# Optimization experiments

Measured on AMD Instinct MI355X. Metric: run time of the kernel, lower is better.

## Reference

```python
import jax, jax.numpy as jnp
import numpy as np

B, N, M = 4, 1024, 3072          # batch, latent (query) len, prefix context len
D, H, DH, L, F = 512, 8, 64, 6, 2048  # dim, heads, dim_head, depth, ff hidden
SCALE = DH ** -0.5


def _ln(x, g, b):
    m = jnp.mean(x, axis=-1, keepdims=True)
    v = jnp.mean(jnp.square(x - m), axis=-1, keepdims=True)
    return (x - m) * jax.lax.rsqrt(v + 1e-5) * g + b


def _heads(t):  # [b, n, h*d] -> [b, h, n, d]
    b, n, _ = t.shape
    return t.reshape(b, n, H, DH).transpose(0, 2, 1, 3)


def _attend(q, k, v):
    # q:[b,h,i,d], k/v:[b,h,j,d]; causal mask triu(j-i+1) as in source
    i, j = q.shape[2], k.shape[2]
    sim = jnp.einsum('bhid,bhjd->bhij', q * SCALE, k)
    mask = jnp.triu(jnp.ones((i, j), dtype=bool), j - i + 1)
    sim = jnp.where(mask, -jnp.finfo(sim.dtype).max, sim)
    attn = jax.nn.softmax(sim, axis=-1)
    out = jnp.einsum('bhij,bhjd->bhid', attn, v)
    return out.transpose(0, 2, 1, 3).reshape(q.shape[0], i, H * DH)


def _ff(x, g, b, w1, w2):
    return jax.nn.gelu(_ln(x, g, b) @ w1, approximate=False) @ w2


def setup_inputs() -> dict:
    key = jax.random.key(0)
    ks = jax.random.split(key, 12)
    rn = lambda k, shape: jax.random.normal(k, shape, dtype=jnp.float32) * 0.02
    return {
        'x': jax.random.normal(ks[0], (B, N, D), jnp.float32),
        'context': jax.random.normal(ks[1], (B, M, D), jnp.float32),
        'pa_norm_g': jnp.ones((D,), jnp.float32), 'pa_norm_b': jnp.zeros((D,), jnp.float32),
        'pa_cnorm_g': jnp.ones((D,), jnp.float32), 'pa_cnorm_b': jnp.zeros((D,), jnp.float32),
        'pa_wq': rn(ks[2], (D, H * DH)), 'pa_wkv': rn(ks[3], (D, 2 * H * DH)),
        'pa_wo': rn(ks[4], (H * DH, D)), 'pa_wo_b': jnp.zeros((D,), jnp.float32),
        'pf_ln_g': jnp.ones((D,), jnp.float32), 'pf_ln_b': jnp.zeros((D,), jnp.float32),
        'pf_w1': rn(ks[5], (D, F)), 'pf_w2': rn(ks[6], (F, D)),
        'sa_ln_g': jnp.ones((L, D), jnp.float32), 'sa_ln_b': jnp.zeros((L, D), jnp.float32),
        'sa_wqkv': rn(ks[7], (L, D, 3 * H * DH)), 'sa_wo': rn(ks[8], (L, H * DH, D)),
        'sf_ln_g': jnp.ones((L, D), jnp.float32), 'sf_ln_b': jnp.zeros((L, D), jnp.float32),
        'sf_w1': rn(ks[9], (L, D, F)), 'sf_w2': rn(ks[10], (L, F, D)),
    }


def reference(x, context, pa_norm_g, pa_norm_b, pa_cnorm_g, pa_cnorm_b,
              pa_wq, pa_wkv, pa_wo, pa_wo_b, pf_ln_g, pf_ln_b, pf_w1, pf_w2,
              sa_ln_g, sa_ln_b, sa_wqkv, sa_wo, sf_ln_g, sf_ln_b, sf_w1, sf_w2):
    # --- CausalPrefixAttention (eval mode: no dropout, context_mask=None) ---
    xn = _ln(x, pa_norm_g, pa_norm_b)
    cn = _ln(context, pa_cnorm_g, pa_cnorm_b)
    q = _heads(xn @ pa_wq)
    k_in, v_in = jnp.split(xn @ pa_wkv, 2, axis=-1)
    k_c, v_c = jnp.split(cn @ pa_wkv, 2, axis=-1)
    k = _heads(jnp.concatenate([k_c, k_in], axis=1))  # [b,h,M+N,d]
    v = _heads(jnp.concatenate([v_c, v_in], axis=1))
    x = _attend(q, k, v) @ pa_wo + pa_wo_b + x
    x = _ff(x, pf_ln_g, pf_ln_b, pf_w1, pf_w2) + x
    # --- depth x (CausalAttention + FeedForward) ---
    for l in range(L):
        xn = _ln(x, sa_ln_g[l], sa_ln_b[l])
        qq, kk, vv = jnp.split(xn @ sa_wqkv[l], 3, axis=-1)
        x = _attend(_heads(qq), _heads(kk), _heads(vv)) @ sa_wo[l] + x
        x = _ff(x, sf_ln_g[l], sf_ln_b[l], sf_w1[l], sf_w2[l]) + x
    return x
```

## Files before the change

### kernel.cpp

```cpp
#include <hip/hip_runtime.h>
#include <hip/hip_bf16.h>
#include <cstdint>
#include <cstddef>

typedef __bf16 bf16;
typedef __attribute__((ext_vector_type(8))) __bf16 bf16x8;
typedef __attribute__((ext_vector_type(4))) __bf16 bf16x4;
typedef __attribute__((ext_vector_type(4))) float f32x4;

constexpr int B_ = 4, QN = 1024, MCTX = 3072, D_ = 512, H_ = 8, DHE = 64, L_ = 6, FF_ = 2048;
constexpr float SCALE_ = 0.125f;

__device__ __forceinline__ f32x4 mfma16(bf16x8 a, bf16x8 b, f32x4 c) {
  return __builtin_amdgcn_mfma_f32_16x16x32_bf16(a, b, c, 0, 0, 0);
}

__device__ __forceinline__ void gl_lds16(const bf16* g, bf16* l) {
  __builtin_amdgcn_global_load_lds((const __attribute__((address_space(1))) void*)g,
                                   (__attribute__((address_space(3))) void*)l, 16, 0, 0);
}

__global__ __launch_bounds__(256) void ln_kernel(const float* __restrict__ x,
                                                 const float* __restrict__ g,
                                                 const float* __restrict__ b,
                                                 bf16* __restrict__ out, int rows) {
  int wid = threadIdx.x >> 6, lane = threadIdx.x & 63;
  int row = blockIdx.x * 4 + wid;
  if (row >= rows) return;
  const float* xr = x + (size_t)row * D_;
  f32x4 a0 = *(const f32x4*)(xr + lane * 8);
  f32x4 a1 = *(const f32x4*)(xr + lane * 8 + 4);
  float s = 0.f;
#pragma unroll
  for (int i = 0; i < 4; i++) { s += a0[i]; s += a1[i]; }
#pragma unroll
  for (int d = 1; d < 64; d <<= 1) s += __shfl_xor(s, d);
  float mean = s * (1.0f / 512.0f);
  float q = 0.f;
#pragma unroll
  for (int i = 0; i < 4; i++) {
    float t0 = a0[i] - mean, t1 = a1[i] - mean;
    q += t0 * t0 + t1 * t1;
  }
#pragma unroll
  for (int d = 1; d < 64; d <<= 1) q += __shfl_xor(q, d);
  float rstd = rsqrtf(q * (1.0f / 512.0f) + 1e-5f);
  f32x4 g0 = *(const f32x4*)(g + lane * 8);
  f32x4 g1 = *(const f32x4*)(g + lane * 8 + 4);
  f32x4 b0 = *(const f32x4*)(b + lane * 8);
  f32x4 b1 = *(const f32x4*)(b + lane * 8 + 4);
  bf16x8 o;
#pragma unroll
  for (int i = 0; i < 4; i++) {
    o[i] = (bf16)((a0[i] - mean) * rstd * g0[i] + b0[i]);
    o[i + 4] = (bf16)((a1[i] - mean) * rstd * g1[i] + b1[i]);
  }
  *(bf16x8*)(out + (size_t)row * D_ + lane * 8) = o;
}

struct WDesc { const float* src; bf16* dst; int K; int N; int tstart; };
struct WPack { WDesc d[30]; int n; };

__global__ __launch_bounds__(256) void wtrans_all(WPack p) {
  __shared__ float tile[64][65];
  const int bid = blockIdx.x;
  int mi = 0;
  for (int i = 1; i < p.n; i++)
    if (p.d[i].tstart <= bid) mi = i;
  const float* src = p.d[mi].src;
  bf16* dst = p.d[mi].dst;
  const int K = p.d[mi].K, N = p.d[mi].N;
  const int lt = bid - p.d[mi].tstart;
  const int ntx = N >> 6;
  const int n0 = (lt % ntx) * 64, k0 = (lt / ntx) * 64;
  const int tx = threadIdx.x, ty = threadIdx.y;
#pragma unroll
  for (int pp = 0; pp < 16; pp++)
    tile[pp * 4 + ty][tx] = src[(size_t)(k0 + pp * 4 + ty) * N + n0 + tx];
  __syncthreads();
#pragma unroll
  for (int pp = 0; pp < 16; pp++)
    dst[(size_t)(n0 + pp * 4 + ty) * K + k0 + tx] = (bf16)tile[tx][pp * 4 + ty];
}

__global__ __launch_bounds__(256) void vtrans_kernel(const bf16* __restrict__ src,
                                                     bf16* __restrict__ vt,
                                                     int Skv, int rstride, int coloff) {
  __shared__ bf16 tile[64][65];
  int tx = threadIdx.x, ty = threadIdx.y;
  int s0 = blockIdx.x * 64, h = blockIdx.y, b = blockIdx.z;
  const bf16* sp = src + (size_t)b * Skv * rstride + coloff + h * 64;
#pragma unroll
  for (int p = 0; p < 16; p++)
    tile[p * 4 + ty][tx] = sp[(size_t)(s0 + p * 4 + ty) * rstride + tx];
  __syncthreads();
  bf16* op = vt + ((size_t)(b * H_ + h) * 64) * Skv;
#pragma unroll
  for (int p = 0; p < 16; p++)
    op[(size_t)(p * 4 + ty) * Skv + s0 + tx] = tile[tx][p * 4 + ty];
}

template <int EPI>
__global__ __launch_bounds__(256) void gemm128(const bf16* __restrict__ A,
                                               const bf16* __restrict__ BT,
                                               void* __restrict__ Cout,
                                               const float* __restrict__ resid,
                                               const float* __restrict__ bias,
                                               int M, int N, int K,
                                               int rpbi, int rpbo, int roff) {
  __shared__ bf16 smA[2][128 * 64];
  __shared__ bf16 smB[2][128 * 64];
  const int tid = threadIdx.x, wid = tid >> 6, lane = tid & 63;
  const int lr = lane & 15, lg = lane >> 4;
  const int tm = blockIdx.y * 128, tn = blockIdx.x * 128;
  const int wr = (wid >> 1) * 64, wc = (wid & 1) * 64;

  const int l3 = lane >> 3;
  const int kslot = ((lane & 7) ^ l3) * 8;
  const bf16* gA[4];
  const bf16* gB[4];
#pragma unroll
  for (int j = 0; j < 4; j++) {
    gA[j] = A + (size_t)(tm + wid * 32 + j * 8 + l3) * K + kslot;
    gB[j] = BT + (size_t)(tn + wid * 32 + j * 8 + l3) * K + kslot;
  }

  f32x4 acc[4][4] = {};
  const int nt = K >> 6;

  auto stage = [&](int bi, int kt) {
#pragma unroll
    for (int j = 0; j < 4; j++) {
      gl_lds16(gA[j] + kt, &smA[bi][(wid * 32 + j * 8) * 64]);
      gl_lds16(gB[j] + kt, &smB[bi][(wid * 32 + j * 8) * 64]);
    }
  };

  stage(0, 0);
  int buf = 0;
  for (int t = 0; t < nt; ++t) {
    asm volatile("s_waitcnt vmcnt(0)" ::: "memory");
    __builtin_amdgcn_s_barrier();
    __builtin_amdgcn_sched_barrier(0);
    if (t + 1 < nt) stage(buf ^ 1, (t + 1) * 64);

    bf16x8 af[4][2], bfr[4][2];
#pragma unroll
    for (int i = 0; i < 4; i++) {
      const int row = wr + i * 16 + lr;
#pragma unroll
      for (int kk = 0; kk < 2; kk++)
        af[i][kk] = *(const bf16x8*)(&smA[buf][row * 64 + (((kk * 4 + lg) ^ (row & 7)) * 8)]);
    }
#pragma unroll
    for (int j = 0; j < 4; j++) {
      const int row = wc + j * 16 + lr;
#pragma unroll
      for (int kk = 0; kk < 2; kk++)
        bfr[j][kk] = *(const bf16x8*)(&smB[buf][row * 64 + (((kk * 4 + lg) ^ (row & 7)) * 8)]);
    }
#pragma unroll
    for (int kk = 0; kk < 2; kk++)
#pragma unroll
      for (int i = 0; i < 4; i++)
#pragma unroll
        for (int j = 0; j < 4; j++)
          acc[i][j] = mfma16(af[i][kk], bfr[j][kk], acc[i][j]);
    buf ^= 1;
  }

#pragma unroll
  for (int i = 0; i < 4; i++) {
#pragma unroll
    for (int r = 0; r < 4; r++) {
      int row = tm + wr + i * 16 + lg * 4 + r;
      int orow = (row / rpbi) * rpbo + (row % rpbi) + roff;
#pragma unroll
      for (int j = 0; j < 4; j++) {
        int col = tn + wc + j * 16 + lr;
        float v = acc[i][j][r];
        if (EPI == 0) {
          ((bf16*)Cout)[(size_t)orow * N + col] = (bf16)v;
        } else if (EPI == 1) {
          float gv = 0.5f * v * (1.0f + erff(v * 0.70710678118f));
          ((bf16*)Cout)[(size_t)orow * N + col] = (bf16)gv;
        } else {
          if (bias) v += bias[col];
          v += resid[(size_t)orow * N + col];
          ((float*)Cout)[(size_t)orow * N + col] = v;
        }
      }
    }
  }
}

template <int EPI>
__global__ __launch_bounds__(256) void gemm64(const bf16* __restrict__ A,
                                              const bf16* __restrict__ BT,
                                              void* __restrict__ Cout,
                                              const float* __restrict__ resid,
                                              const float* __restrict__ bias,
                                              int M, int N, int K,
                                              int rpbi, int rpbo, int roff) {
  __shared__ bf16 smA[3][64 * 64];
  __shared__ bf16 smB[3][64 * 64];
  const int tid = threadIdx.x, wid = tid >> 6, lane = tid & 63;
  const int lr = lane & 15, lg = lane >> 4;
  const int tm = blockIdx.y * 64, tn = blockIdx.x * 64;
  const int wr = (wid >> 1) * 32, wc = (wid & 1) * 32;

  const int l3 = lane >> 3;
  const int kslot = ((lane & 7) ^ l3) * 8;
  const int row0 = 2 * wid * 8 + l3;
  const bf16* gA0 = A + (size_t)(tm + row0) * K + kslot;
  const bf16* gA1 = A + (size_t)(tm + row0 + 8) * K + kslot;
  const bf16* gB0 = BT + (size_t)(tn + row0) * K + kslot;
  const bf16* gB1 = BT + (size_t)(tn + row0 + 8) * K + kslot;

  f32x4 acc[2][2] = {};
  const int nt = K >> 6;

  auto stage = [&](int bi, int kt) {
    gl_lds16(gA0 + kt, &smA[bi][(2 * wid) * 512]);
    gl_lds16(gA1 + kt, &smA[bi][(2 * wid + 1) * 512]);
    gl_lds16(gB0 + kt, &smB[bi][(2 * wid) * 512]);
    gl_lds16(gB1 + kt, &smB[bi][(2 * wid + 1) * 512]);
  };

  stage(0, 0);
  if (nt > 1) stage(1, 64);

  for (int t = 0; t < nt; ++t) {
    const int bi = t % 3;
    if (t + 1 < nt) {
      asm volatile("s_waitcnt vmcnt(4)" ::: "memory");
    } else {
      asm volatile("s_waitcnt vmcnt(0)" ::: "memory");
    }
    __builtin_amdgcn_s_barrier();
    __builtin_amdgcn_sched_barrier(0);
    if (t + 2 < nt) stage((t + 2) % 3, (t + 2) * 64);

    bf16x8 af[2][2], bfr[2][2];
#pragma unroll
    for (int i = 0; i < 2; i++) {
      const int row = wr + i * 16 + lr;
#pragma unroll
      for (int kk = 0; kk < 2; kk++)
        af[i][kk] = *(const bf16x8*)(&smA[bi][row * 64 + (((kk * 4 + lg) ^ (row & 7)) * 8)]);
    }
#pragma unroll
    for (int j = 0; j < 2; j++) {
      const int row = wc + j * 16 + lr;
#pragma unroll
      for (int kk = 0; kk < 2; kk++)
        bfr[j][kk] = *(const bf16x8*)(&smB[bi][row * 64 + (((kk * 4 + lg) ^ (row & 7)) * 8)]);
    }
#pragma unroll
    for (int kk = 0; kk < 2; kk++)
#pragma unroll
      for (int i = 0; i < 2; i++)
#pragma unroll
        for (int j = 0; j < 2; j++)
          acc[i][j] = mfma16(af[i][kk], bfr[j][kk], acc[i][j]);
  }

#pragma unroll
  for (int i = 0; i < 2; i++) {
#pragma unroll
    for (int r = 0; r < 4; r++) {
      int row = tm + wr + i * 16 + lg * 4 + r;
      int orow = (row / rpbi) * rpbo + (row % rpbi) + roff;
#pragma unroll
      for (int j = 0; j < 2; j++) {
        int col = tn + wc + j * 16 + lr;
        float v = acc[i][j][r];
        if (EPI == 0) {
          ((bf16*)Cout)[(size_t)orow * N + col] = (bf16)v;
        } else if (EPI == 1) {
          float gv = 0.5f * v * (1.0f + erff(v * 0.70710678118f));
          ((bf16*)Cout)[(size_t)orow * N + col] = (bf16)gv;
        } else {
          if (bias) v += bias[col];
          v += resid[(size_t)orow * N + col];
          ((float*)Cout)[(size_t)orow * N + col] = v;
        }
      }
    }
  }
}

template <int NSPLIT>
__global__ __launch_bounds__(256) void attn_kernel(const bf16* __restrict__ q, int qstride,
                                                   const bf16* __restrict__ k, int kstride,
                                                   const bf16* __restrict__ vt,
                                                   bf16* __restrict__ out,
                                                   bf16* __restrict__ po,
                                                   float* __restrict__ pm,
                                                   float* __restrict__ pl,
                                                   int Skv, int Moff, int spllen) {
  __shared__ bf16 kls[2][4096];
  __shared__ bf16 vls[2][4096];
  __shared__ bf16 pls[4][1024];

  const int tid = threadIdx.x, wid = tid >> 6, lane = tid & 63;
  const int lr = lane & 15, lg = lane >> 4, lg4 = lg * 4;
  const int b = blockIdx.z, h = blockIdx.y;
  const int qblk = blockIdx.x / NSPLIT;
  const int split = blockIdx.x % NSPLIT;
  const int q0b = qblk * 64;
  const int q0w = q0b + wid * 16;
  const int kv_lo = split * spllen;

  int jhi_blk = Moff + q0b + 63;
  if (jhi_blk > Skv - 1) jhi_blk = Skv - 1;
  int hi = kv_lo + spllen;
  if (hi > jhi_blk + 1) hi = jhi_blk + 1;
  const int ntl = (hi > kv_lo) ? ((hi - kv_lo + 63) >> 6) : 0;

  if (NSPLIT > 1 && ntl == 0) {
    size_t rb = ((size_t)split * B_ * H_ + (size_t)b * H_ + h) * QN + q0w;
#pragma unroll
    for (int f = 0; f < 4; f++)
#pragma unroll
      for (int r = 0; r < 4; r++) po[(rb + lg4 + r) * 64 + f * 16 + lr] = (bf16)0.f;
    if (lg == 0) { pm[rb + lr] = -3e38f; pl[rb + lr] = 0.f; }
    return;
  }

  const int ss = (tid >> 6) & 1;
  const int sel = ss * 32 + ((tid >> 4) & 3) * 8;
  const int srow0 = (tid >> 7) * 16 + (tid & 15);
  const bf16* kbase = k + (size_t)b * Skv * kstride + h * DHE + sel;
  const bf16* vbase = vt + (size_t)((b * H_ + h) * DHE) * Skv + sel;

  const bf16* qp = q + (size_t)(b * QN + q0w + lr) * qstride + h * DHE;
  bf16x8 qa0 = *(const bf16x8*)(qp + lg * 8);
  bf16x8 qa1 = *(const bf16x8*)(qp + 32 + lg * 8);
#pragma unroll
  for (int i = 0; i < 8; i++) {
    qa0[i] = (bf16)((float)qa0[i] * SCALE_);
    qa1[i] = (bf16)((float)qa1[i] * SCALE_);
  }

  f32x4 o[4] = {};
  float mr = -3e38f, lrun = 0.f;

  auto stage = [&](int bi, int j0) {
    gl_lds16(kbase + (size_t)(j0 + srow0) * kstride, &kls[bi][wid * 512]);
    gl_lds16(kbase + (size_t)(j0 + srow0 + 32) * kstride, &kls[bi][2048 + wid * 512]);
    gl_lds16(vbase + (size_t)srow0 * Skv + j0, &vls[bi][wid * 512]);
    gl_lds16(vbase + (size_t)(srow0 + 32) * Skv + j0, &vls[bi][2048 + wid * 512]);
  };

  stage(0, kv_lo);
  __syncthreads();
  int buf = 0;
  bf16* pw = &pls[wid][0];

  for (int t = 0; t < ntl; ++t) {
    const int j0 = kv_lo + t * 64;
    if (t + 1 < ntl) stage(buf ^ 1, j0 + 64);
    const bf16* kbp = &kls[buf][0];
    const bf16* vbp = &vls[buf][0];

    f32x4 sv[4];
    __builtin_amdgcn_s_setprio(1);
#pragma unroll
    for (int kg = 0; kg < 4; kg++) {
      bf16x8 k0 = *(const bf16x8*)(kbp + (kg * 128 + lane) * 8);
      bf16x8 k1 = *(const bf16x8*)(kbp + (kg * 128 + 64 + lane) * 8);
      f32x4 z = {0.f, 0.f, 0.f, 0.f};
      z = mfma16(k0, qa0, z);
      z = mfma16(k1, qa1, z);
      sv[kg] = z;
    }
    __builtin_amdgcn_s_setprio(0);
    const bool full = (j0 + 63 <= Moff + q0w);
    if (!full) {
      const int limq = Moff + q0w + lr;
#pragma unroll
      for (int kg = 0; kg < 4; kg++)
#pragma unroll
        for (int r = 0; r < 4; r++)
          if (j0 + kg * 16 + lg4 + r > limq) sv[kg][r] = -3e38f;
    }
    float pmax = sv[0][0];
#pragma unroll
    for (int kg = 0; kg < 4; kg++)
#pragma unroll
      for (int r = 0; r < 4; r++) pmax = fmaxf(pmax, sv[kg][r]);
    pmax = fmaxf(pmax, __shfl_xor(pmax, 16));
    pmax = fmaxf(pmax, __shfl_xor(pmax, 32));
    if (__any(pmax > mr + 8.f)) {
      float mn = fmaxf(mr, pmax);
      float scl = __expf(mr - mn);
      mr = mn;
      lrun *= scl;
      float c0 = __shfl(scl, lg4 + 0), c1 = __shfl(scl, lg4 + 1);
      float c2 = __shfl(scl, lg4 + 2), c3 = __shfl(scl, lg4 + 3);
#pragma unroll
      for (int f = 0; f < 4; f++) {
        o[f][0] *= c0; o[f][1] *= c1; o[f][2] *= c2; o[f][3] *= c3;
      }
    }
    float rsum = 0.f;
#pragma unroll
    for (int kg = 0; kg < 4; kg++) {
      float p0 = __expf(sv[kg][0] - mr);
      float p1 = __expf(sv[kg][1] - mr);
      float p2 = __expf(sv[kg][2] - mr);
      float p3 = __expf(sv[kg][3] - mr);
      rsum += (p0 + p1) + (p2 + p3);
      bf16x4 pk = {(bf16)p0, (bf16)p1, (bf16)p2, (bf16)p3};
      const int k8 = kg * 2 + (lg >> 1);
      *(bf16x4*)(pw + ((k8 >> 2) * 64 + (k8 & 3) * 16 + lr) * 8 + (lg & 1) * 4) = pk;
    }
    rsum += __shfl_xor(rsum, 16);
    rsum += __shfl_xor(rsum, 32);
    lrun += rsum;
    bf16x8 pa0 = *(const bf16x8*)(pw + lane * 8);
    bf16x8 pa1 = *(const bf16x8*)(pw + (64 + lane) * 8);
    __builtin_amdgcn_s_setprio(1);
#pragma unroll
    for (int f = 0; f < 4; f++) {
      bf16x8 v0 = *(const bf16x8*)(vbp + (f * 128 + lane) * 8);
      bf16x8 v1 = *(const bf16x8*)(vbp + (f * 128 + 64 + lane) * 8);
      o[f] = mfma16(pa0, v0, o[f]);
      o[f] = mfma16(pa1, v1, o[f]);
    }
    __builtin_amdgcn_s_setprio(0);
    __syncthreads();
    buf ^= 1;
  }

  if (NSPLIT == 1) {
    float linv = 1.0f / lrun;
    float li[4];
#pragma unroll
    for (int r = 0; r < 4; r++) li[r] = __shfl(linv, lg4 + r);
#pragma unroll
    for (int f = 0; f < 4; f++)
#pragma unroll
      for (int r = 0; r < 4; r++)
        out[(size_t)(b * QN + q0w + lg4 + r) * D_ + h * DHE + f * 16 + lr] =
            (bf16)(o[f][r] * li[r]);
  } else {
    size_t rb = ((size_t)split * B_ * H_ + (size_t)b * H_ + h) * QN + q0w;
#pragma unroll
    for (int f = 0; f < 4; f++)
#pragma unroll
      for (int r = 0; r < 4; r++)
        po[(rb + lg4 + r) * 64 + f * 16 + lr] = (bf16)o[f][r];
    if (lg == 0) { pm[rb + lr] = mr; pl[rb + lr] = lrun; }
  }
}

template <int NSPLIT>
__global__ __launch_bounds__(256) void attn_combine(const bf16* __restrict__ po,
                                                    const float* __restrict__ pm,
                                                    const float* __restrict__ pl,
                                                    bf16* __restrict__ out) {
  constexpr int TOT = B_ * H_ * QN;
  const int wid = threadIdx.x >> 6, lane = threadIdx.x & 63;
  const int row = blockIdx.x * 4 + wid;
  float mv[NSPLIT], lv[NSPLIT];
  float mstar = -3e38f;
#pragma unroll
  for (int s = 0; s < NSPLIT; s++) {
    mv[s] = pm[s * TOT + row];
    lv[s] = pl[s * TOT + row];
    mstar = fmaxf(mstar, mv[s]);
  }
  float lstar = 0.f, acc = 0.f;
#pragma unroll
  for (int s = 0; s < NSPLIT; s++) {
    float w = __expf(mv[s] - mstar);
    lstar += lv[s] * w;
    acc += (float)po[((size_t)s * TOT + row) * 64 + lane] * w;
  }
  const int b = row >> 13, hq = row & 8191, h = hq >> 10, qq = hq & 1023;
  out[((size_t)b * QN + qq) * D_ + h * DHE + lane] = (bf16)(acc / lstar);
}

static void launch_gemm(hipStream_t st, int epi, const bf16* A, const bf16* BT, void* C,
                        const float* res, const float* bias,
                        int M, int N, int K, int rpbi, int rpbo, int roff) {
  if (N >= 1024) {
    dim3 grid(N / 128, M / 128), blk(256, 1, 1);
    switch (epi) {
      case 0:
        hipLaunchKernelGGL(HIP_KERNEL_NAME(gemm128<0>), grid, blk, 0, st, A, BT, C, res, bias, M, N, K, rpbi, rpbo, roff);
        break;
      case 1:
        hipLaunchKernelGGL(HIP_KERNEL_NAME(gemm128<1>), grid, blk, 0, st, A, BT, C, res, bias, M, N, K, rpbi, rpbo, roff);
        break;
      default:
        hipLaunchKernelGGL(HIP_KERNEL_NAME(gemm128<2>), grid, blk, 0, st, A, BT, C, res, bias, M, N, K, rpbi, rpbo, roff);
        break;
    }
    return;
  }
  dim3 grid(N / 64, M / 64), blk(256, 1, 1);
  switch (epi) {
    case 0:
      hipLaunchKernelGGL(HIP_KERNEL_NAME(gemm64<0>), grid, blk, 0, st, A, BT, C, res, bias, M, N, K, rpbi, rpbo, roff);
      break;
    case 1:
      hipLaunchKernelGGL(HIP_KERNEL_NAME(gemm64<1>), grid, blk, 0, st, A, BT, C, res, bias, M, N, K, rpbi, rpbo, roff);
      break;
    default:
      hipLaunchKernelGGL(HIP_KERNEL_NAME(gemm64<2>), grid, blk, 0, st, A, BT, C, res, bias, M, N, K, rpbi, rpbo, roff);
      break;
  }
}

extern "C" void kernel_launch(void* const* d_in, const int* in_sizes, int n_in,
                              void* d_out, int out_size, void* d_ws, size_t ws_size,
                              hipStream_t stream) {
  const float* x       = (const float*)d_in[0];
  const float* ctx     = (const float*)d_in[1];
  const float* pa_ng   = (const float*)d_in[2];
  const float* pa_nb   = (const float*)d_in[3];
  const float* pa_cg   = (const float*)d_in[4];
  const float* pa_cb   = (const float*)d_in[5];
  const float* pa_wq   = (const float*)d_in[6];
  const float* pa_wkv  = (const float*)d_in[7];
  const float* pa_wo   = (const float*)d_in[8];
  const float* pa_wob  = (const float*)d_in[9];
  const float* pf_g    = (const float*)d_in[10];
  const float* pf_b    = (const float*)d_in[11];
  const float* pf_w1   = (const float*)d_in[12];
  const float* pf_w2   = (const float*)d_in[13];
  const float* sa_g    = (const float*)d_in[14];
  const float* sa_b    = (const float*)d_in[15];
  const float* sa_wqkv = (const float*)d_in[16];
  const float* sa_wo   = (const float*)d_in[17];
  const float* sf_g    = (const float*)d_in[18];
  const float* sf_b    = (const float*)d_in[19];
  const float* sf_w1   = (const float*)d_in[20];
  const float* sf_w2   = (const float*)d_in[21];
  float* xo = (float*)d_out;

  char* ws = (char*)d_ws;
  size_t off = 0;
  auto alloc = [&](size_t bytes) -> char* {
    char* p = ws + off;
    off += (bytes + 255) & ~(size_t)255;
    return p;
  };

  bf16* wqT    = (bf16*)alloc((size_t)512 * 512 * 2);
  bf16* wkvT   = (bf16*)alloc((size_t)1024 * 512 * 2);
  bf16* woT    = (bf16*)alloc((size_t)512 * 512 * 2);
  bf16* w1T    = (bf16*)alloc((size_t)2048 * 512 * 2);
  bf16* w2T    = (bf16*)alloc((size_t)512 * 2048 * 2);
  bf16* saqkvT = (bf16*)alloc((size_t)L_ * 1536 * 512 * 2);
  bf16* sawoT  = (bf16*)alloc((size_t)L_ * 512 * 512 * 2);
  bf16* sfw1T  = (bf16*)alloc((size_t)L_ * 2048 * 512 * 2);
  bf16* sfw2T  = (bf16*)alloc((size_t)L_ * 512 * 2048 * 2);
  bf16* xn    = (bf16*)alloc((size_t)4096 * 512 * 2);
  bf16* reg1  = (bf16*)alloc((size_t)12288 * 512 * 2);
  bf16* qb    = (bf16*)alloc((size_t)4096 * 512 * 2);
  bf16* reg2  = (bf16*)alloc((size_t)B_ * 4096 * 1024 * 2);
  bf16* vtb   = (bf16*)alloc((size_t)B_ * H_ * 64 * 4096 * 2);
  bf16* attnb = (bf16*)alloc((size_t)4096 * 512 * 2);
  constexpr int NSPL = 4;
  constexpr int TOTR = B_ * H_ * QN;
  bf16* po = (bf16*)alloc((size_t)NSPL * TOTR * 64 * 2);
  float* pmb = (float*)alloc((size_t)NSPL * TOTR * 4);
  float* plb = (float*)alloc((size_t)NSPL * TOTR * 4);
  const bool use_split = (off <= ws_size);
  bf16* cn = reg1;
  bf16* qkvb = reg1;
  bf16* kvb = reg2;
  bf16* ffh = reg2;
  (void)in_sizes; (void)n_in; (void)out_size;

  WPack wp;
  int nt_acc = 0, wi = 0;
  auto addw = [&](const float* s, bf16* d, int K, int N) {
    wp.d[wi].src = s; wp.d[wi].dst = d; wp.d[wi].K = K; wp.d[wi].N = N;
    wp.d[wi].tstart = nt_acc;
    nt_acc += (N / 64) * (K / 64);
    wi++;
  };
  addw(pa_wq, wqT, 512, 512);
  addw(pa_wkv, wkvT, 512, 1024);
  addw(pa_wo, woT, 512, 512);
  addw(pf_w1, w1T, 512, 2048);
  addw(pf_w2, w2T, 2048, 512);
  for (int l = 0; l < L_; l++) {
    addw(sa_wqkv + (size_t)l * 512 * 1536, saqkvT + (size_t)l * 1536 * 512, 512, 1536);
    addw(sa_wo + (size_t)l * 512 * 512, sawoT + (size_t)l * 512 * 512, 512, 512);
    addw(sf_w1 + (size_t)l * 512 * 2048, sfw1T + (size_t)l * 2048 * 512, 512, 2048);
    addw(sf_w2 + (size_t)l * 2048 * 512, sfw2T + (size_t)l * 512 * 2048, 2048, 512);
  }
  wp.n = wi;
  wtrans_all<<<nt_acc, dim3(64, 4, 1), 0, stream>>>(wp);

  ln_kernel<<<1024, 256, 0, stream>>>(x, pa_ng, pa_nb, xn, 4096);
  ln_kernel<<<3072, 256, 0, stream>>>(ctx, pa_cg, pa_cb, cn, 12288);
  launch_gemm(stream, 0, xn, wqT, qb, nullptr, nullptr, 4096, 512, 512, 4096, 4096, 0);
  launch_gemm(stream, 0, cn, wkvT, kvb, nullptr, nullptr, 12288, 1024, 512, 3072, 4096, 0);
  launch_gemm(stream, 0, xn, wkvT, kvb, nullptr, nullptr, 4096, 1024, 512, 1024, 4096, 3072);
  vtrans_kernel<<<dim3(64, H_, B_), dim3(64, 4, 1), 0, stream>>>(kvb, vtb, 4096, 1024, 512);
  if (use_split) {
    hipLaunchKernelGGL(HIP_KERNEL_NAME(attn_kernel<NSPL>), dim3((QN / 64) * NSPL, H_, B_), dim3(256), 0,
                       stream, qb, 512, kvb, 1024, vtb, attnb, po, pmb, plb, 4096, MCTX, 1024);
    hipLaunchKernelGGL(HIP_KERNEL_NAME(attn_combine<NSPL>), dim3(TOTR / 4), dim3(256), 0,
                       stream, po, pmb, plb, attnb);
  } else {
    hipLaunchKernelGGL(HIP_KERNEL_NAME(attn_kernel<1>), dim3(QN / 64, H_, B_), dim3(256), 0,
                       stream, qb, 512, kvb, 1024, vtb, attnb, po, pmb, plb, 4096, MCTX, 4096);
  }
  launch_gemm(stream, 2, attnb, woT, xo, x, pa_wob, 4096, 512, 512, 4096, 4096, 0);
  ln_kernel<<<1024, 256, 0, stream>>>(xo, pf_g, pf_b, xn, 4096);
  launch_gemm(stream, 1, xn, w1T, ffh, nullptr, nullptr, 4096, 2048, 512, 4096, 4096, 0);
  launch_gemm(stream, 2, ffh, w2T, xo, xo, nullptr, 4096, 512, 2048, 4096, 4096, 0);

  for (int l = 0; l < L_; l++) {
    ln_kernel<<<1024, 256, 0, stream>>>(xo, sa_g + l * 512, sa_b + l * 512, xn, 4096);
    launch_gemm(stream, 0, xn, saqkvT + (size_t)l * 1536 * 512, qkvb, nullptr, nullptr,
                4096, 1536, 512, 4096, 4096, 0);
    vtrans_kernel<<<dim3(16, H_, B_), dim3(64, 4, 1), 0, stream>>>(qkvb, vtb, 1024, 1536, 1024);
    if (use_split) {
      hipLaunchKernelGGL(HIP_KERNEL_NAME(attn_kernel<2>), dim3((QN / 64) * 2, H_, B_), dim3(256), 0,
                         stream, qkvb, 1536, qkvb + 512, 1536, vtb, attnb, po, pmb, plb, 1024, 0, 512);
      hipLaunchKernelGGL(HIP_KERNEL_NAME(attn_combine<2>), dim3(TOTR / 4), dim3(256), 0,
                         stream, po, pmb, plb, attnb);
    } else {
      hipLaunchKernelGGL(HIP_KERNEL_NAME(attn_kernel<1>), dim3(QN / 64, H_, B_), dim3(256), 0,
                         stream, qkvb, 1536, qkvb + 512, 1536, vtb, attnb, po, pmb, plb, 1024, 0, 1024);
    }
    launch_gemm(stream, 2, attnb, sawoT + (size_t)l * 512 * 512, xo, xo, nullptr,
                4096, 512, 512, 4096, 4096, 0);
    ln_kernel<<<1024, 256, 0, stream>>>(xo, sf_g + l * 512, sf_b + l * 512, xn, 4096);
    launch_gemm(stream, 1, xn, sfw1T + (size_t)l * 2048 * 512, ffh, nullptr, nullptr,
                4096, 2048, 512, 4096, 4096, 0);
    launch_gemm(stream, 2, ffh, sfw2T + (size_t)l * 512 * 2048, xo, xo, nullptr,
                4096, 512, 2048, 4096, 4096, 0);
  }
}
```

Before: 910.8 us.

## Fuse V transpose and Q/KV projection routing into GEMM epilogues, use exp2 softmax

Removes the separate vtrans kernels. The QKV and context-KV GEMM epilogues now write V directly in transposed per-head layout and scatter K/V into the combined KV buffer. The query-side Q and KV projections are merged into one N=1536 GEMM by concatenating the wq and wkv weights. Softmax switches to exp2 with log2(e) folded into the Q scale, and the rescale threshold is raised to match. The self-attention split factor also changes from 2 to NSPL. The trade-off is extra kernel launches saved against scattered 8-byte transposed stores in the epilogue, and the weight concatenation must be set up correctly elsewhere.

Measured after the change: 927.5 us. About the same (+1.8%).

```diff
diff --git a/kernel.cpp b/kernel.cpp
--- a/kernel.cpp
+++ b/kernel.cpp
@@ -9,7 +9,7 @@
 typedef __attribute__((ext_vector_type(4))) float f32x4;
 
 constexpr int B_ = 4, QN = 1024, MCTX = 3072, D_ = 512, H_ = 8, DHE = 64, L_ = 6, FF_ = 2048;
-constexpr float SCALE_ = 0.125f;
+constexpr float SCL2_ = 0.18033688011f;
 
 __device__ __forceinline__ f32x4 mfma16(bf16x8 a, bf16x8 b, f32x4 c) {
   return __builtin_amdgcn_mfma_f32_16x16x32_bf16(a, b, c, 0, 0, 0);
@@ -83,31 +83,15 @@
     dst[(size_t)(n0 + pp * 4 + ty) * K + k0 + tx] = (bf16)tile[tx][pp * 4 + ty];
 }
 
-__global__ __launch_bounds__(256) void vtrans_kernel(const bf16* __restrict__ src,
-                                                     bf16* __restrict__ vt,
-                                                     int Skv, int rstride, int coloff) {
-  __shared__ bf16 tile[64][65];
-  int tx = threadIdx.x, ty = threadIdx.y;
-  int s0 = blockIdx.x * 64, h = blockIdx.y, b = blockIdx.z;
-  const bf16* sp = src + (size_t)b * Skv * rstride + coloff + h * 64;
-#pragma unroll
-  for (int p = 0; p < 16; p++)
-    tile[p * 4 + ty][tx] = sp[(size_t)(s0 + p * 4 + ty) * rstride + tx];
-  __syncthreads();
-  bf16* op = vt + ((size_t)(b * H_ + h) * 64) * Skv;
-#pragma unroll
-  for (int p = 0; p < 16; p++)
-    op[(size_t)(p * 4 + ty) * Skv + s0 + tx] = tile[tx][p * 4 + ty];
-}
-
 template <int EPI>
 __global__ __launch_bounds__(256) void gemm128(const bf16* __restrict__ A,
                                                const bf16* __restrict__ BT,
-                                               void* __restrict__ Cout,
+                                               void* __restrict__ C0,
+                                               void* __restrict__ C1,
+                                               void* __restrict__ C2,
                                                const float* __restrict__ resid,
                                                const float* __restrict__ bias,
-                                               int M, int N, int K,
-                                               int rpbi, int rpbo, int roff) {
+                                               int M, int N, int K, int vstr) {
   __shared__ bf16 smA[2][128 * 64];
   __shared__ bf16 smB[2][128 * 64];
   const int tid = threadIdx.x, wid = tid >> 6, lane = tid & 63;
@@ -171,37 +155,70 @@
 
 #pragma unroll
   for (int i = 0; i < 4; i++) {
-#pragma unroll
-    for (int r = 0; r < 4; r++) {
-      int row = tm + wr + i * 16 + lg * 4 + r;
-      int orow = (row / rpbi) * rpbo + (row % rpbi) + roff;
-#pragma unroll
-      for (int j = 0; j < 4; j++) {
-        int col = tn + wc + j * 16 + lr;
-        float v = acc[i][j][r];
-        if (EPI == 0) {
-          ((bf16*)Cout)[(size_t)orow * N + col] = (bf16)v;
-        } else if (EPI == 1) {
+    const int row = tm + wr + i * 16 + lg * 4;
+#pragma unroll
+    for (int j = 0; j < 4; j++) {
+      const int col = tn + wc + j * 16 + lr;
+      if (EPI == 1) {
+#pragma unroll
+        for (int r = 0; r < 4; r++) {
+          float v = acc[i][j][r];
           float gv = 0.5f * v * (1.0f + erff(v * 0.70710678118f));
-          ((bf16*)Cout)[(size_t)orow * N + col] = (bf16)gv;
+          ((bf16*)C0)[(size_t)(row + r) * N + col] = (bf16)gv;
+        }
+      } else if (EPI == 3) {
+        if (col < 512) {
+#pragma unroll
+          for (int r = 0; r < 4; r++)
+            ((bf16*)C0)[(size_t)(row + r) * 512 + col] = (bf16)acc[i][j][r];
+        } else if (col < 1024) {
+          const int orow = (row >> 10) * 4096 + (row & 1023) + 3072;
+#pragma unroll
+          for (int r = 0; r < 4; r++)
+            ((bf16*)C1)[(size_t)(orow + r) * 1024 + (col - 512)] = (bf16)acc[i][j][r];
         } else {
-          if (bias) v += bias[col];
-          v += resid[(size_t)orow * N + col];
-          ((float*)Cout)[(size_t)orow * N + col] = v;
+          const int cc = col - 1024, hh = cc >> 6, dh = cc & 63;
+          const int bb = row >> 10, s = (row & 1023) + 3072;
+          bf16x4 pk = {(bf16)acc[i][j][0], (bf16)acc[i][j][1],
+                       (bf16)acc[i][j][2], (bf16)acc[i][j][3]};
+          *(bf16x4*)&((bf16*)C2)[((size_t)(bb * 8 + hh) * 64 + dh) * vstr + s] = pk;
+        }
+      } else if (EPI == 4) {
+        if (col < 1024) {
+#pragma unroll
+          for (int r = 0; r < 4; r++)
+            ((bf16*)C0)[(size_t)(row + r) * 1536 + col] = (bf16)acc[i][j][r];
+        } else {
+          const int cc = col - 1024, hh = cc >> 6, dh = cc & 63;
+          const int bb = row >> 10, s = row & 1023;
+          bf16x4 pk = {(bf16)acc[i][j][0], (bf16)acc[i][j][1],
+                       (bf16)acc[i][j][2], (bf16)acc[i][j][3]};
+          *(bf16x4*)&((bf16*)C2)[((size_t)(bb * 8 + hh) * 64 + dh) * vstr + s] = pk;
+        }
+      } else if (EPI == 5) {
+        const int bq = row / 3072, s = row - bq * 3072;
+        if (col < 512) {
+          const int orow = bq * 4096 + s;
+#pragma unroll
+          for (int r = 0; r < 4; r++)
+            ((bf16*)C1)[(size_t)(orow + r) * 1024 + col] = (bf16)acc[i][j][r];
+        } else {
+          const int cc = col - 512, hh = cc >> 6, dh = cc & 63;
+          bf16x4 pk = {(bf16)acc[i][j][0], (bf16)acc[i][j][1],
+                       (bf16)acc[i][j][2], (bf16)acc[i][j][3]};
+          *(bf16x4*)&((bf16*)C2)[((size_t)(bq * 8 + hh) * 64 + dh) * vstr + s] = pk;
         }
       }
     }
   }
 }
 
-template <int EPI>
-__global__ __launch_bounds__(256) void gemm64(const bf16* __restrict__ A,
-                                              const bf16* __restrict__ BT,
-                                              void* __restrict__ Cout,
-                                              const float* __restrict__ resid,
-                                              const float* __restrict__ bias,
-                                              int M, int N, int K,
-                                              int rpbi, int rpbo, int roff) {
+__global__ __launch_bounds__(256) void gemm64_res(const bf16* __restrict__ A,
+                                                  const bf16* __restrict__ BT,
+                                                  float* __restrict__ Cout,
+                                                  const float* __restrict__ resid,
+                                                  const float* __restrict__ bias,
+                                                  int M, int N, int K) {
   __shared__ bf16 smA[3][64 * 64];
   __shared__ bf16 smB[3][64 * 64];
   const int tid = threadIdx.x, wid = tid >> 6, lane = tid & 63;
@@ -270,21 +287,13 @@
 #pragma unroll
     for (int r = 0; r < 4; r++) {
       int row = tm + wr + i * 16 + lg * 4 + r;
-      int orow = (row / rpbi) * rpbo + (row % rpbi) + roff;
 #pragma unroll
       for (int j = 0; j < 2; j++) {
         int col = tn + wc + j * 16 + lr;
         float v = acc[i][j][r];
-        if (EPI == 0) {
-          ((bf16*)Cout)[(size_t)orow * N + col] = (bf16)v;
-        } else if (EPI == 1) {
-          float gv = 0.5f * v * (1.0f + erff(v * 0.70710678118f));
-          ((bf16*)Cout)[(size_t)orow * N + col] = (bf16)gv;
-        } else {
-          if (bias) v += bias[col];
-          v += resid[(size_t)orow * N + col];
-          ((float*)Cout)[(size_t)orow * N + col] = v;
-        }
+        if (bias) v += bias[col];
+        v += resid[(size_t)row * N + col];
+        Cout[(size_t)row * N + col] = v;
       }
     }
   }
@@ -339,8 +348,8 @@
   bf16x8 qa1 = *(const bf16x8*)(qp + 32 + lg * 8);
 #pragma unroll
   for (int i = 0; i < 8; i++) {
-    qa0[i] = (bf16)((float)qa0[i] * SCALE_);
-    qa1[i] = (bf16)((float)qa1[i] * SCALE_);
+    qa0[i] = (bf16)((float)qa0[i] * SCL2_);
+    qa1[i] = (bf16)((float)qa1[i] * SCL2_);
   }
 
   f32x4 o[4] = {};
@@ -385,16 +394,16 @@
         for (int r = 0; r < 4; r++)
           if (j0 + kg * 16 + lg4 + r > limq) sv[kg][r] = -3e38f;
     }
-    float pmax = sv[0][0];
+    float mk[4];
 #pragma unroll
     for (int kg = 0; kg < 4; kg++)
-#pragma unroll
-      for (int r = 0; r < 4; r++) pmax = fmaxf(pmax, sv[kg][r]);
+      mk[kg] = fmaxf(fmaxf(sv[kg][0], sv[kg][1]), fmaxf(sv[kg][2], sv[kg][3]));
+    float pmax = fmaxf(fmaxf(mk[0], mk[1]), fmaxf(mk[2], mk[3]));
     pmax = fmaxf(pmax, __shfl_xor(pmax, 16));
     pmax = fmaxf(pmax, __shfl_xor(pmax, 32));
-    if (__any(pmax > mr + 8.f)) {
+    if (__any(pmax > mr + 11.5f)) {
       float mn = fmaxf(mr, pmax);
-      float scl = __expf(mr - mn);
+      float scl = exp2f(mr - mn);
       mr = mn;
       lrun *= scl;
       float c0 = __shfl(scl, lg4 + 0), c1 = __shfl(scl, lg4 + 1);
@@ -407,10 +416,10 @@
     float rsum = 0.f;
 #pragma unroll
     for (int kg = 0; kg < 4; kg++) {
-      float p0 = __expf(sv[kg][0] - mr);
-      float p1 = __expf(sv[kg][1] - mr);
-      float p2 = __expf(sv[kg][2] - mr);
-      float p3 = __expf(sv[kg][3] - mr);
+      float p0 = exp2f(sv[kg][0] - mr);
+      float p1 = exp2f(sv[kg][1] - mr);
+      float p2 = exp2f(sv[kg][2] - mr);
+      float p3 = exp2f(sv[kg][3] - mr);
       rsum += (p0 + p1) + (p2 + p3);
       bf16x4 pk = {(bf16)p0, (bf16)p1, (bf16)p2, (bf16)p3};
       const int k8 = kg * 2 + (lg >> 1);
@@ -475,44 +484,12 @@
   float lstar = 0.f, acc = 0.f;
 #pragma unroll
   for (int s = 0; s < NSPLIT; s++) {
-    float w = __expf(mv[s] - mstar);
+    float w = exp2f(mv[s] - mstar);
     lstar += lv[s] * w;
     acc += (float)po[((size_t)s * TOT + row) * 64 + lane] * w;
   }
   const int b = row >> 13, hq = row & 8191, h = hq >> 10, qq = hq & 1023;
   out[((size_t)b * QN + qq) * D_ + h * DHE + lane] = (bf16)(acc / lstar);
-}
-
-static void launch_gemm(hipStream_t st, int epi, const bf16* A, const bf16* BT, void* C,
-                        const float* res, const float* bias,
-                        int M, int N, int K, int rpbi, int rpbo, int roff) {
-  if (N >= 1024) {
-    dim3 grid(N / 128, M / 128), blk(256, 1, 1);
-    switch (epi) {
-      case 0:
-        hipLaunchKernelGGL(HIP_KERNEL_NAME(gemm128<0>), grid, blk, 0, st, A, BT, C, res, bias, M, N, K, rpbi, rpbo, roff);
-        break;
-      case 1:
-        hipLaunchKernelGGL(HIP_KERNEL_NAME(gemm128<1>), grid, blk, 0, st, A, BT, C, res, bias, M, N, K, rpbi, rpbo, roff);
-        break;
-      default:
-        hipLaunchKernelGGL(HIP_KERNEL_NAME(gemm128<2>), grid, blk, 0, st, A, BT, C, res, bias, M, N, K, rpbi, rpbo, roff);
-        break;
-    }
-    return;
-  }
-  dim3 grid(N / 64, M / 64), blk(256, 1, 1);
-  switch (epi) {
-    case 0:
-      hipLaunchKernelGGL(HIP_KERNEL_NAME(gemm64<0>), grid, blk, 0, st, A, BT, C, res, bias, M, N, K, rpbi, rpbo, roff);
-      break;
-    case 1:
-      hipLaunchKernelGGL(HIP_KERNEL_NAME(gemm64<1>), grid, blk, 0, st, A, BT, C, res, bias, M, N, K, rpbi, rpbo, roff);
-      break;
-    default:
-      hipLaunchKernelGGL(HIP_KERNEL_NAME(gemm64<2>), grid, blk, 0, st, A, BT, C, res, bias, M, N, K, rpbi, rpbo, roff);
-      break;
-  }
 }
 
 extern "C" void kernel_launch(void* const* d_in, const int* in_sizes, int n_in,
@@ -601,10 +578,10 @@
 
   ln_kernel<<<1024, 256, 0, stream>>>(x, pa_ng, pa_nb, xn, 4096);
   ln_kernel<<<3072, 256, 0, stream>>>(ctx, pa_cg, pa_cb, cn, 12288);
-  launch_gemm(stream, 0, xn, wqT, qb, nullptr, nullptr, 4096, 512, 512, 4096, 4096, 0);
-  launch_gemm(stream, 0, cn, wkvT, kvb, nullptr, nullptr, 12288, 1024, 512, 3072, 4096, 0);
-  launch_gemm(stream, 0, xn, wkvT, kvb, nullptr, nullptr, 4096, 1024, 512, 1024, 4096, 3072);
-  vtrans_kernel<<<dim3(64, H_, B_), dim3(64, 4, 1), 0, stream>>>(kvb, vtb, 4096, 1024, 512);
+  hipLaunchKernelGGL(HIP_KERNEL_NAME(gemm128<5>), dim3(1024 / 128, 12288 / 128), dim3(256), 0,
+                     stream, cn, wkvT, nullptr, kvb, vtb, nullptr, nullptr, 12288, 1024, 512, 4096);
+  hipLaunchKernelGGL(HIP_KERNEL_NAME(gemm128<3>), dim3(1536 / 128, 4096 / 128), dim3(256), 0,
+                     stream, xn, wqT, qb, kvb, vtb, nullptr, nullptr, 4096, 1536, 512, 4096);
   if (use_split) {
     hipLaunchKernelGGL(HIP_KERNEL_NAME(attn_kernel<NSPL>), dim3((QN / 64) * NSPL, H_, B_), dim3(256), 0,
                        stream, qb, 512, kvb, 1024, vtb, attnb, po, pmb, plb, 4096, MCTX, 1024);
@@ -614,31 +591,33 @@
     hipLaunchKernelGGL(HIP_KERNEL_NAME(attn_kernel<1>), dim3(QN / 64, H_, B_), dim3(256), 0,
                        stream, qb, 512, kvb, 1024, vtb, attnb, po, pmb, plb, 4096, MCTX, 4096);
   }
-  launch_gemm(stream, 2, attnb, woT, xo, x, pa_wob, 4096, 512, 512, 4096, 4096, 0);
+  gemm64_res<<<dim3(512 / 64, 4096 / 64), 256, 0, stream>>>(attnb, woT, xo, x, pa_wob, 4096, 512, 512);
   ln_kernel<<<1024, 256, 0, stream>>>(xo, pf_g, pf_b, xn, 4096);
-  launch_gemm(stream, 1, xn, w1T, ffh, nullptr, nullptr, 4096, 2048, 512, 4096, 4096, 0);
-  launch_gemm(stream, 2, ffh, w2T, xo, xo, nullptr, 4096, 512, 2048, 4096, 4096, 0);
+  hipLaunchKernelGGL(HIP_KERNEL_NAME(gemm128<1>), dim3(2048 / 128, 4096 / 128), dim3(256), 0,
+                     stream, xn, w1T, ffh, nullptr, nullptr, nullptr, nullptr, 4096, 2048, 512, 0);
+  gemm64_res<<<dim3(512 / 64, 4096 / 64), 256, 0, stream>>>(ffh, w2T, xo, xo, nullptr, 4096, 512, 2048);
 
   for (int l = 0; l < L_; l++) {
     ln_kernel<<<1024, 256, 0, stream>>>(xo, sa_g + l * 512, sa_b + l * 512, xn, 4096);
-    launch_gemm(stream, 0, xn, saqkvT + (size_t)l * 1536 * 512, qkvb, nullptr, nullptr,
-                4096, 1536, 512, 4096, 4096, 0);
-    vtrans_kernel<<<dim3(16, H_, B_), dim3(64, 4, 1), 0, stream>>>(qkvb, vtb, 1024, 1536, 1024);
+    hipLaunchKernelGGL(HIP_KERNEL_NAME(gemm128<4>), dim3(1536 / 128, 4096 / 128), dim3(256), 0,
+                       stream, xn, saqkvT + (size_t)l * 1536 * 512, qkvb, nullptr, vtb,
+                       nullptr, nullptr, 4096, 1536, 512, 1024);
     if (use_split) {
-      hipLaunchKernelGGL(HIP_KERNEL_NAME(attn_kernel<2>), dim3((QN / 64) * 2, H_, B_), dim3(256), 0,
-                         stream, qkvb, 1536, qkvb + 512, 1536, vtb, attnb, po, pmb, plb, 1024, 0, 512);
-      hipLaunchKernelGGL(HIP_KERNEL_NAME(attn_combine<2>), dim3(TOTR / 4), dim3(256), 0,
+      hipLaunchKernelGGL(HIP_KERNEL_NAME(attn_kernel<NSPL>), dim3((QN / 64) * NSPL, H_, B_), dim3(256), 0,
+                         stream, qkvb, 1536, qkvb + 512, 1536, vtb, attnb, po, pmb, plb, 1024, 0, 256);
+      hipLaunchKernelGGL(HIP_KERNEL_NAME(attn_combine<NSPL>), dim3(TOTR / 4), dim3(256), 0,
                          stream, po, pmb, plb, attnb);
     } else {
       hipLaunchKernelGGL(HIP_KERNEL_NAME(attn_kernel<1>), dim3(QN / 64, H_, B_), dim3(256), 0,
                          stream, qkvb, 1536, qkvb + 512, 1536, vtb, attnb, po, pmb, plb, 1024, 0, 1024);
     }
-    launch_gemm(stream, 2, attnb, sawoT + (size_t)l * 512 * 512, xo, xo, nullptr,
-                4096, 512, 512, 4096, 4096, 0);
+    gemm64_res<<<dim3(512 / 64, 4096 / 64), 256, 0, stream>>>(attnb, sawoT + (size_t)l * 512 * 512,
+                                                              xo, xo, nullptr, 4096, 512, 512);
     ln_kernel<<<1024, 256, 0, stream>>>(xo, sf_g + l * 512, sf_b + l * 512, xn, 4096);
-    launch_gemm(stream, 1, xn, sfw1T + (size_t)l * 2048 * 512, ffh, nullptr, nullptr,
-                4096, 2048, 512, 4096, 4096, 0);
-    launch_gemm(stream, 2, ffh, sfw2T + (size_t)l * 512 * 2048, xo, xo, nullptr,
-                4096, 512, 2048, 4096, 4096, 0);
-  }
-}
+    hipLaunchKernelGGL(HIP_KERNEL_NAME(gemm128<1>), dim3(2048 / 128, 4096 / 128), dim3(256), 0,
+                       stream, xn, sfw1T + (size_t)l * 2048 * 512, ffh, nullptr, nullptr,
+                       nullptr, nullptr, 4096, 2048, 512, 0);
+    gemm64_res<<<dim3(512 / 64, 4096 / 64), 256, 0, stream>>>(ffh, sfw2T + (size_t)l * 512 * 2048,
+                                                              xo, xo, nullptr, 4096, 512, 2048);
+  }
+}
```
